# Optimization experiments

Measured on AMD Instinct MI355X. Metric: run time of the kernel, lower is better.

## Reference

```python
import jax, jax.numpy as jnp
import numpy as np

N = 100000
E = 1600000
D_IN = 128
D_H = 128
D_OUT = 40


def setup_inputs() -> dict:
    key = jax.random.key(0)
    ks = jax.random.split(key, 16)
    x = jax.random.normal(ks[0], (N, D_IN), dtype=jnp.float32)
    edge_src = jax.random.randint(ks[1], (E,), 0, N, dtype=jnp.int32)
    edge_dst = jax.random.randint(ks[2], (E,), 0, N, dtype=jnp.int32)

    def glorot(k, shape):
        fan_in, fan_out = shape[1], shape[0]
        lim = jnp.sqrt(6.0 / (fan_in + fan_out)).astype(jnp.float32)
        return jax.random.uniform(k, shape, jnp.float32, -lim, lim)

    # SAGEConv params: Wl acts on aggregated neighbors, Wr on root, plus bias.
    Wl0 = glorot(ks[3], (D_H, D_IN)); Wr0 = glorot(ks[4], (D_H, D_IN)); b0 = jnp.zeros((D_H,), jnp.float32)
    Wl1 = glorot(ks[5], (D_H, D_H));  Wr1 = glorot(ks[6], (D_H, D_H));  b1 = jnp.zeros((D_H,), jnp.float32)
    Wl2 = glorot(ks[7], (D_OUT, D_H)); Wr2 = glorot(ks[8], (D_OUT, D_H)); b2 = jnp.zeros((D_OUT,), jnp.float32)
    return {"x": x, "edge_src": edge_src, "edge_dst": edge_dst,
            "Wl0": Wl0, "Wr0": Wr0, "b0": b0,
            "Wl1": Wl1, "Wr1": Wr1, "b1": b1,
            "Wl2": Wl2, "Wr2": Wr2, "b2": b2}


def _mean_aggregate(x, edge_src, edge_dst, inv_deg):
    # adj_t @ x with mean reduce: sum neighbor feats into dst, divide by degree
    agg = jax.ops.segment_sum(x[edge_src], edge_dst, num_segments=N)
    return agg * inv_deg


def _sage_conv(x, edge_src, edge_dst, inv_deg, Wl, Wr, b):
    agg = _mean_aggregate(x, edge_src, edge_dst, inv_deg)
    return agg @ Wl.T + x @ Wr.T + b


def reference(x, edge_src, edge_dst, Wl0, Wr0, b0, Wl1, Wr1, b1, Wl2, Wr2, b2):
    deg = jax.ops.segment_sum(jnp.ones((E,), jnp.float32), edge_dst, num_segments=N)
    inv_deg = (1.0 / jnp.maximum(deg, 1.0))[:, None]  # [N,1]
    h = _sage_conv(x, edge_src, edge_dst, inv_deg, Wl0, Wr0, b0)
    h = jax.nn.relu(h)  # dropout is identity in eval mode
    h = _sage_conv(h, edge_src, edge_dst, inv_deg, Wl1, Wr1, b1)
    h = jax.nn.relu(h)
    h = _sage_conv(h, edge_src, edge_dst, inv_deg, Wl2, Wr2, b2)
    return jax.nn.log_softmax(h, axis=-1)
```

## Files before the change

kernel.cpp:

```cpp
#include <hip/hip_runtime.h>
#include <hip/hip_fp16.h>
#include <math.h>

#define NN 100000
#define NE 1600000
#define D 128
#define DOUT 40
#define NBUCK 391
#define CHUNK 4096
#define NCHUNK 391
#define LSTR 136

typedef _Float16 half8v __attribute__((ext_vector_type(8)));
typedef __attribute__((ext_vector_type(4))) float f32x4;

__device__ __forceinline__ unsigned packh(float a, float b) {
  return (unsigned)__half_as_ushort(__float2half_rn(a)) |
         ((unsigned)__half_as_ushort(__float2half_rn(b)) << 16);
}
__device__ __forceinline__ unsigned char f2fp8(float v) {
  return (unsigned char)(__builtin_amdgcn_cvt_pk_fp8_f32(v, v, 0, 0) & 0xff);
}
#define CVT2(u, s) __builtin_amdgcn_cvt_pk_f32_fp8((int)(u), s)
#define ACCR(v) { auto q = CVT2((v).x, 0); a[0] += q[0]; a[1] += q[1];   \
  q = CVT2((v).x, 1); a[2] += q[0];  a[3] += q[1];                        \
  q = CVT2((v).y, 0); a[4] += q[0];  a[5] += q[1];                        \
  q = CVT2((v).y, 1); a[6] += q[0];  a[7] += q[1];                        \
  q = CVT2((v).z, 0); a[8] += q[0];  a[9] += q[1];                        \
  q = CVT2((v).z, 1); a[10] += q[0]; a[11] += q[1];                       \
  q = CVT2((v).w, 0); a[12] += q[0]; a[13] += q[1];                       \
  q = CVT2((v).w, 1); a[14] += q[0]; a[15] += q[1]; }
#define ACCR8(v) { auto q = CVT2((v).x, 0); a[0] += q[0]; a[1] += q[1];  \
  q = CVT2((v).x, 1); a[2] += q[0]; a[3] += q[1];                         \
  q = CVT2((v).y, 0); a[4] += q[0]; a[5] += q[1];                         \
  q = CVT2((v).y, 1); a[6] += q[0]; a[7] += q[1]; }

__global__ __launch_bounds__(256) void cvt_kernel(const float* __restrict__ in,
                                                  _Float16* __restrict__ outh,
                                                  unsigned char* __restrict__ out8) {
  int i = (blockIdx.x * 256 + threadIdx.x) * 8;
  float4 v0 = *(const float4*)(in + i);
  float4 v1 = *(const float4*)(in + i + 4);
  uint4 oh;
  oh.x = packh(v0.x, v0.y);
  oh.y = packh(v0.z, v0.w);
  oh.z = packh(v1.x, v1.y);
  oh.w = packh(v1.z, v1.w);
  *(uint4*)(outh + i) = oh;
  unsigned w0 = __builtin_amdgcn_cvt_pk_fp8_f32(v0.x, v0.y, 0, 0);
  w0 = __builtin_amdgcn_cvt_pk_fp8_f32(v0.z, v0.w, w0, 1);
  unsigned w1 = __builtin_amdgcn_cvt_pk_fp8_f32(v1.x, v1.y, 0, 0);
  w1 = __builtin_amdgcn_cvt_pk_fp8_f32(v1.z, v1.w, w1, 1);
  *(uint2*)(out8 + i) = make_uint2(w0, w1);
}

__global__ __launch_bounds__(256) void bucket_hist_kernel(const int* __restrict__ dst,
                                                          int* __restrict__ bucket_cnt) {
  __shared__ int bc[NBUCK];
  int t = threadIdx.x;
  for (int i = t; i < NBUCK; i += 256) bc[i] = 0;
  __syncthreads();
  int e_base = blockIdx.x * CHUNK;
#pragma unroll
  for (int j = 0; j < 16; ++j) {
    int e = e_base + j * 256 + t;
    if (e < NE) atomicAdd(&bc[dst[e] >> 8], 1);
  }
  __syncthreads();
  for (int i = t; i < NBUCK; i += 256)
    if (bc[i]) atomicAdd(&bucket_cnt[i], bc[i]);
}

__global__ __launch_bounds__(512) void bucket_scan_kernel(const int* __restrict__ bucket_cnt,
                                                          int* __restrict__ bucket_base,
                                                          int* __restrict__ bucket_cursor) {
  __shared__ int s[512];
  int t = threadIdx.x;
  int c = (t < NBUCK) ? bucket_cnt[t] : 0;
  s[t] = c;
  __syncthreads();
  for (int off = 1; off < 512; off <<= 1) {
    int v = (t >= off) ? s[t - off] : 0;
    __syncthreads();
    s[t] += v;
    __syncthreads();
  }
  if (t < NBUCK) {
    int b = s[t] - c;
    bucket_base[t] = b;
    bucket_cursor[t] = b;
  }
  if (t == NBUCK) bucket_base[NBUCK] = s[NBUCK - 1];
}

__global__ __launch_bounds__(256) void binned_scatter_kernel(const int* __restrict__ src,
                                                             const int* __restrict__ dst,
                                                             int* __restrict__ bucket_cursor,
                                                             unsigned* __restrict__ pairs) {
  __shared__ int lcnt[NBUCK];
  __shared__ int lscan[NBUCK];
  __shared__ int gb[NBUCK];
  __shared__ unsigned ebuf[CHUNK];
  __shared__ unsigned short bbuf[CHUNK];
  int t = threadIdx.x;
  int e_base = blockIdx.x * CHUNK;
  for (int i = t; i < NBUCK; i += 256) lcnt[i] = 0;
  __syncthreads();

  int myb[16], myrank[16];
  unsigned mye[16];
#pragma unroll
  for (int j = 0; j < 16; ++j) {
    int e = e_base + j * 256 + t;
    if (e < NE) {
      int d = dst[e];
      mye[j] = (unsigned)src[e] | ((unsigned)(d & 255) << 24);
      myb[j] = d >> 8;
      myrank[j] = atomicAdd(&lcnt[d >> 8], 1);
    } else {
      myb[j] = -1;
    }
  }
  __syncthreads();

  lscan[t] = lcnt[t];
  if (256 + t < NBUCK) lscan[256 + t] = lcnt[256 + t];
  __syncthreads();
  for (int off = 1; off < 512; off <<= 1) {
    int v0 = (t >= off) ? lscan[t - off] : 0;
    int v1 = 0;
    int i1 = 256 + t;
    if (i1 < NBUCK) v1 = lscan[i1 - off];
    __syncthreads();
    if (t >= off) lscan[t] += v0;
    if (i1 < NBUCK) lscan[i1] += v1;
    __syncthreads();
  }

#pragma unroll
  for (int j = 0; j < 16; ++j)
    if (myb[j] >= 0) {
      int b = myb[j];
      int lpos = lscan[b] - lcnt[b] + myrank[j];
      ebuf[lpos] = mye[j];
      bbuf[lpos] = (unsigned short)b;
    }
  for (int i = t; i < NBUCK; i += 256)
    if (lcnt[i] > 0) gb[i] = atomicAdd(&bucket_cursor[i], lcnt[i]);
  __syncthreads();

  int chunk_n = min(CHUNK, NE - e_base);
  for (int s2 = t; s2 < chunk_n; s2 += 256) {
    int b = bbuf[s2];
    int g = gb[b] + (s2 - (lscan[b] - lcnt[b]));
    pairs[g] = ebuf[s2];
  }
}

__global__ __launch_bounds__(256) void bucket_build_kernel(const unsigned* __restrict__ pairs,
                                                           const int* __restrict__ bucket_base,
                                                           int* __restrict__ row_start,
                                                           int* __restrict__ nbr,
                                                           float* __restrict__ inv_deg) {
  __shared__ int cnt[256], loc[256], cur[256];
  int b = blockIdx.x;
  int t = threadIdx.x;
  int nbase = b << 8;
  int e0 = bucket_base[b], e1 = bucket_base[b + 1];
  cnt[t] = 0;
  __syncthreads();
  for (int e = e0 + t; e < e1; e += 256) {
    int d = (int)(pairs[e] >> 24);
    atomicAdd(&cnt[d], 1);
  }
  __syncthreads();
  loc[t] = cnt[t];
  __syncthreads();
  for (int off = 1; off < 256; off <<= 1) {
    int v = (t >= off) ? loc[t - off] : 0;
    __syncthreads();
    loc[t] += v;
    __syncthreads();
  }
  int excl = loc[t] - cnt[t];
  int node = nbase + t;
  if (node < NN) {
    row_start[node] = e0 + excl;
    inv_deg[node] = 1.0f / (float)(cnt[t] > 1 ? cnt[t] : 1);
  }
  cur[t] = excl;
  if (b == NBUCK - 1 && t == 0) row_start[NN] = NE;
  __syncthreads();
  for (int e = e0 + t; e < e1; e += 256) {
    unsigned pr = pairs[e];
    int d = (int)(pr >> 24);
    int p = atomicAdd(&cur[d], 1);
    nbr[e0 + p] = (int)(pr & 0xFFFFFFu);
  }
}

__global__ __launch_bounds__(256) void agg_kernel(const unsigned char* __restrict__ X8,
                                                  _Float16* __restrict__ out,
                                                  const int* __restrict__ row_start,
                                                  const int* __restrict__ nbr,
                                                  const float* __restrict__ inv_deg) {
  int g = blockIdx.x * 32 + (threadIdx.x >> 3);
  int ln = threadIdx.x & 7;
  if (g >= NN) return;
  int p0 = row_start[g];
  int p1 = row_start[g + 1];
  const uint4* base = (const uint4*)X8;
  float a[16];
#pragma unroll
  for (int i = 0; i < 16; ++i) a[i] = 0.f;
  int p = p0;
  for (; p + 3 < p1; p += 4) {
    int s0 = nbr[p], s1 = nbr[p + 1], s2 = nbr[p + 2], s3 = nbr[p + 3];
    uint4 v0 = base[(size_t)s0 * 8 + ln];
    uint4 v1 = base[(size_t)s1 * 8 + ln];
    uint4 v2 = base[(size_t)s2 * 8 + ln];
    uint4 v3 = base[(size_t)s3 * 8 + ln];
    ACCR(v0) ACCR(v1) ACCR(v2) ACCR(v3)
  }
  for (; p < p1; ++p) {
    uint4 v = base[(size_t)nbr[p] * 8 + ln];
    ACCR(v)
  }
  float id = inv_deg[g];
  uint4 o0, o1;
  o0.x = packh(a[0] * id, a[1] * id);
  o0.y = packh(a[2] * id, a[3] * id);
  o0.z = packh(a[4] * id, a[5] * id);
  o0.w = packh(a[6] * id, a[7] * id);
  o1.x = packh(a[8] * id, a[9] * id);
  o1.y = packh(a[10] * id, a[11] * id);
  o1.z = packh(a[12] * id, a[13] * id);
  o1.w = packh(a[14] * id, a[15] * id);
  uint4* ob = (uint4*)out;
  ob[(size_t)g * 16 + ln * 2] = o0;
  ob[(size_t)g * 16 + ln * 2 + 1] = o1;
}

__global__ __launch_bounds__(64) void prep_w_kernel(const float* __restrict__ Wl,
                                                    const float* __restrict__ Wr,
                                                    half8v* __restrict__ P) {
  int s = blockIdx.x >> 3;
  int n = blockIdx.x & 7;
  int l = threadIdx.x;
  int k0 = s * 32 + (l >> 4) * 8;
  int c = n * 16 + (l & 15);
  const float* W = (k0 < 128) ? Wl : Wr;
  int kb = (k0 < 128) ? k0 : k0 - 128;
  half8v h;
#pragma unroll
  for (int i = 0; i < 8; ++i) h[i] = (_Float16)W[c * 128 + kb + i];
  P[blockIdx.x * 64 + l] = h;
}

__global__ __launch_bounds__(64) void prep_wy2_kernel(const float* __restrict__ Wl,
                                                      const float* __restrict__ Wr,
                                                      half8v* __restrict__ P) {
  int s = blockIdx.x / 5;
  int n = blockIdx.x % 5;
  int l = threadIdx.x;
  int k0 = s * 32 + (l >> 4) * 8;
  int c = n * 16 + (l & 15);
  const float* W = (c < DOUT) ? Wl : Wr;
  int row = (c < DOUT) ? c : c - DOUT;
  half8v h;
#pragma unroll
  for (int i = 0; i < 8; ++i) h[i] = (_Float16)W[row * 128 + k0 + i];
  P[blockIdx.x * 64 + l] = h;
}

__global__ __launch_bounds__(256) void mfma_gemm_kernel(
    const _Float16* __restrict__ A, const _Float16* __restrict__ H,
    const half8v* __restrict__ B, const float* __restrict__ bias,
    _Float16* __restrict__ out, unsigned char* __restrict__ out8) {
  __shared__ _Float16 AH[2][128][LSTR];

  int t = threadIdx.x;
  int w = t >> 6, l = t & 63;
  int R0 = blockIdx.x * 128;
  int lc = l & 15;
  int lg = l >> 4;

#pragma unroll
  for (int i = 0; i < 8; ++i) {
    int u = t + 256 * i;
    int row = u >> 4, seg = u & 15;
    int gr = R0 + row;
    uint4 va = make_uint4(0, 0, 0, 0), vh = va;
    if (gr < NN) {
      va = *(const uint4*)(A + (size_t)gr * D + seg * 8);
      vh = *(const uint4*)(H + (size_t)gr * D + seg * 8);
    }
    *(uint4*)&AH[0][row][seg * 8] = va;
    *(uint4*)&AH[1][row][seg * 8] = vh;
  }
  __syncthreads();

  f32x4 acc[2][8];
#pragma unroll
  for (int m = 0; m < 2; ++m)
#pragma unroll
    for (int n = 0; n < 8; ++n) acc[m][n] = (f32x4){0.f, 0.f, 0.f, 0.f};

#pragma unroll
  for (int s = 0; s < 8; ++s) {
    int half = s >> 2;
    int koff = (s & 3) * 32;
    half8v bh[8];
#pragma unroll
    for (int n = 0; n < 8; ++n) bh[n] = B[(s * 8 + n) * 64 + l];
    half8v ah[2];
#pragma unroll
    for (int m = 0; m < 2; ++m) {
      int r = w * 32 + m * 16 + lc;
      ah[m] = *(const half8v*)&AH[half][r][koff + lg * 8];
    }
#pragma unroll
    for (int n = 0; n < 8; ++n)
#pragma unroll
      for (int m = 0; m < 2; ++m)
        acc[m][n] = __builtin_amdgcn_mfma_f32_16x16x32_f16(ah[m], bh[n], acc[m][n], 0, 0, 0);
  }

  float bcol[8];
#pragma unroll
  for (int n = 0; n < 8; ++n) bcol[n] = bias[n * 16 + lc];
#pragma unroll
  for (int m = 0; m < 2; ++m)
#pragma unroll
    for (int n = 0; n < 8; ++n) {
      int col = n * 16 + lc;
#pragma unroll
      for (int j = 0; j < 4; ++j) {
        int gr = R0 + w * 32 + m * 16 + lg * 4 + j;
        if (gr < NN) {
          float v = fmaxf(acc[m][n][j] + bcol[n], 0.f);
          out[(size_t)gr * D + col] = (_Float16)v;
          if (out8) out8[(size_t)gr * D + col] = f2fp8(v);
        }
      }
    }
}

__global__ __launch_bounds__(256) void mfma_y2_kernel(
    const _Float16* __restrict__ H, const half8v* __restrict__ B,
    const float* __restrict__ b2,
    unsigned char* __restrict__ yl8, float* __restrict__ yr) {
  __shared__ _Float16 Hs[128][LSTR];

  int t = threadIdx.x;
  int w = t >> 6, l = t & 63;
  int R0 = blockIdx.x * 128;
  int lc = l & 15;
  int lg = l >> 4;

#pragma unroll
  for (int i = 0; i < 8; ++i) {
    int u = t + 256 * i;
    int row = u >> 4, seg = u & 15;
    int gr = R0 + row;
    uint4 v = make_uint4(0, 0, 0, 0);
    if (gr < NN) v = *(const uint4*)(H + (size_t)gr * D + seg * 8);
    *(uint4*)&Hs[row][seg * 8] = v;
  }
  __syncthreads();

  f32x4 acc[2][5];
#pragma unroll
  for (int m = 0; m < 2; ++m)
#pragma unroll
    for (int n = 0; n < 5; ++n) acc[m][n] = (f32x4){0.f, 0.f, 0.f, 0.f};

#pragma unroll
  for (int s = 0; s < 4; ++s) {
    int koff = s * 32;
    half8v bh[5];
#pragma unroll
    for (int n = 0; n < 5; ++n) bh[n] = B[(s * 5 + n) * 64 + l];
    half8v ah[2];
#pragma unroll
    for (int m = 0; m < 2; ++m) {
      int r = w * 32 + m * 16 + lc;
      ah[m] = *(const half8v*)&Hs[r][koff + lg * 8];
    }
#pragma unroll
    for (int n = 0; n < 5; ++n)
#pragma unroll
      for (int m = 0; m < 2; ++m)
        acc[m][n] = __builtin_amdgcn_mfma_f32_16x16x32_f16(ah[m], bh[n], acc[m][n], 0, 0, 0);
  }

#pragma unroll
  for (int m = 0; m < 2; ++m)
#pragma unroll
    for (int n = 0; n < 5; ++n) {
      int col = n * 16 + lc;
#pragma unroll
      for (int j = 0; j < 4; ++j) {
        int gr = R0 + w * 32 + m * 16 + lg * 4 + j;
        if (gr < NN) {
          float v = acc[m][n][j];
          if (col < DOUT) {
            yl8[(size_t)gr * 48 + col] = f2fp8(v);
          } else {
            if (col < 48) yl8[(size_t)gr * 48 + col] = 0;
            yr[(size_t)gr * DOUT + (col - DOUT)] = v + b2[col - DOUT];
          }
        }
      }
    }
}

__global__ __launch_bounds__(256) void agg_out_kernel(const unsigned char* __restrict__ yl8,
                                                      const float* __restrict__ yr,
                                                      const int* __restrict__ row_start,
                                                      const int* __restrict__ nbr,
                                                      const float* __restrict__ inv_deg,
                                                      float* __restrict__ out) {
  int g = blockIdx.x * 32 + (threadIdx.x >> 3);
  int ln = threadIdx.x & 7;
  if (g >= NN) return;
  int lnc = (ln < 6) ? ln : 5;
  int p0 = row_start[g];
  int p1 = row_start[g + 1];
  const uint2* base = (const uint2*)yl8;
  float a[8];
#pragma unroll
  for (int i = 0; i < 8; ++i) a[i] = 0.f;
  int p = p0;
  for (; p + 3 < p1; p += 4) {
    int s0 = nbr[p], s1 = nbr[p + 1], s2 = nbr[p + 2], s3 = nbr[p + 3];
    uint2 v0 = base[(size_t)s0 * 6 + lnc];
    uint2 v1 = base[(size_t)s1 * 6 + lnc];
    uint2 v2 = base[(size_t)s2 * 6 + lnc];
    uint2 v3 = base[(size_t)s3 * 6 + lnc];
    ACCR8(v0) ACCR8(v1) ACCR8(v2) ACCR8(v3)
  }
  for (; p < p1; ++p) {
    uint2 v = base[(size_t)nbr[p] * 6 + lnc];
    ACCR8(v)
  }
  float id = inv_deg[g];
  float z[8];
#pragma unroll
  for (int i = 0; i < 8; ++i) z[i] = a[i] * id;
  bool valid = (ln < 5);
  if (valid) {
    float4 r0 = *(const float4*)(yr + (size_t)g * DOUT + ln * 8);
    float4 r1 = *(const float4*)(yr + (size_t)g * DOUT + ln * 8 + 4);
    z[0] += r0.x; z[1] += r0.y; z[2] += r0.z; z[3] += r0.w;
    z[4] += r1.x; z[5] += r1.y; z[6] += r1.z; z[7] += r1.w;
  }
  float zm = -INFINITY;
  if (valid)
#pragma unroll
    for (int i = 0; i < 8; ++i) zm = fmaxf(zm, z[i]);
#pragma unroll
  for (int off = 1; off < 8; off <<= 1) zm = fmaxf(zm, __shfl_xor(zm, off, 8));
  float ssum = 0.f;
  if (valid)
#pragma unroll
    for (int i = 0; i < 8; ++i) ssum += expf(z[i] - zm);
#pragma unroll
  for (int off = 1; off < 8; off <<= 1) ssum += __shfl_xor(ssum, off, 8);
  float lse = zm + logf(ssum);
  if (valid) {
    float4 o0 = make_float4(z[0] - lse, z[1] - lse, z[2] - lse, z[3] - lse);
    float4 o1 = make_float4(z[4] - lse, z[5] - lse, z[6] - lse, z[7] - lse);
    *(float4*)(out + (size_t)g * DOUT + ln * 8) = o0;
    *(float4*)(out + (size_t)g * DOUT + ln * 8 + 4) = o1;
  }
}

extern "C" void kernel_launch(void* const* d_in, const int* in_sizes, int n_in,
                              void* d_out, int out_size, void* d_ws, size_t ws_size,
                              hipStream_t stream) {
  const float* x   = (const float*)d_in[0];
  const int* esrc  = (const int*)d_in[1];
  const int* edst  = (const int*)d_in[2];
  const float* Wl0 = (const float*)d_in[3];
  const float* Wr0 = (const float*)d_in[4];
  const float* b0  = (const float*)d_in[5];
  const float* Wl1 = (const float*)d_in[6];
  const float* Wr1 = (const float*)d_in[7];
  const float* b1  = (const float*)d_in[8];
  const float* Wl2 = (const float*)d_in[9];
  const float* Wr2 = (const float*)d_in[10];
  const float* b2  = (const float*)d_in[11];
  float* out = (float*)d_out;

  char* ws = (char*)d_ws;
  size_t off = 0;
  auto carve = [&](size_t bytes) -> char* {
    char* p = ws + off;
    off = (off + bytes + 255) & ~(size_t)255;
    return p;
  };
  int* bucket_cnt    = (int*)carve((size_t)NBUCK * 4);
  int* bucket_base   = (int*)carve((size_t)(NBUCK + 1) * 4);
  int* bucket_cursor = (int*)carve((size_t)NBUCK * 4);
  int* row_start     = (int*)carve((size_t)(NN + 1) * 4);
  int* nbr           = (int*)carve((size_t)NE * 4);
  float* inv_deg     = (float*)carve((size_t)NN * 4);
  unsigned* pairs    = (unsigned*)carve((size_t)NE * 4);
  half8v* B0         = (half8v*)carve((size_t)64 * 64 * 16);
  half8v* B1         = (half8v*)carve((size_t)64 * 64 * 16);
  half8v* By2        = (half8v*)carve((size_t)20 * 64 * 16);
  _Float16* xb   = (_Float16*)carve((size_t)NN * D * 2);
  unsigned char* x8    = (unsigned char*)carve((size_t)NN * D);
  _Float16* bufA = (_Float16*)carve((size_t)NN * D * 2);
  _Float16* bufB = (_Float16*)carve((size_t)NN * D * 2);
  unsigned char* bufB8 = (unsigned char*)carve((size_t)NN * D);
  _Float16* bufC = (_Float16*)carve((size_t)NN * D * 2);
  unsigned char* yl8   = (unsigned char*)carve((size_t)NN * 48);
  float* yr      = (float*)carve((size_t)NN * DOUT * 4);
  if (off > ws_size) return;

  const int GRID_AGG = (NN + 31) / 32;
  const int GRID_GEMM = (NN + 127) / 128;
  const int GRID_CVT = NN * D / 8 / 256;
  const int GRID_AO = (NN + 31) / 32;

  hipMemsetAsync(bucket_cnt, 0, (size_t)NBUCK * 4, stream);
  bucket_hist_kernel<<<NCHUNK, 256, 0, stream>>>(edst, bucket_cnt);
  bucket_scan_kernel<<<1, 512, 0, stream>>>(bucket_cnt, bucket_base, bucket_cursor);
  binned_scatter_kernel<<<NCHUNK, 256, 0, stream>>>(esrc, edst, bucket_cursor, pairs);
  bucket_build_kernel<<<NBUCK, 256, 0, stream>>>(pairs, bucket_base, row_start, nbr, inv_deg);

  cvt_kernel<<<GRID_CVT, 256, 0, stream>>>(x, xb, x8);
  prep_w_kernel<<<64, 64, 0, stream>>>(Wl0, Wr0, B0);
  prep_w_kernel<<<64, 64, 0, stream>>>(Wl1, Wr1, B1);
  prep_wy2_kernel<<<20, 64, 0, stream>>>(Wl2, Wr2, By2);

  agg_kernel<<<GRID_AGG, 256, 0, stream>>>(x8, bufA, row_start, nbr, inv_deg);
  mfma_gemm_kernel<<<GRID_GEMM, 256, 0, stream>>>(bufA, xb, B0, b0, bufB, bufB8);
  agg_kernel<<<GRID_AGG, 256, 0, stream>>>(bufB8, bufA, row_start, nbr, inv_deg);
  mfma_gemm_kernel<<<GRID_GEMM, 256, 0, stream>>>(bufA, bufB, B1, b1, bufC, nullptr);
  mfma_y2_kernel<<<GRID_GEMM, 256, 0, stream>>>(bufC, By2, b2, yl8, yr);
  agg_out_kernel<<<GRID_AO, 256, 0, stream>>>(yl8, yr, row_start, nbr, inv_deg, out);
}
```

Before: 261.7 us.

## Load GEMM A-fragments directly from global and stage outputs through LDS for coalesced stores

Both MFMA kernels stop staging the input tiles in shared memory and instead load each lane's A fragments straight from global memory, clamping row indices so no bounds check is needed. The epilogues now write results into an LDS tile and then store them with vectorised, coalesced row writes; the fp8 copy is derived from the staged fp16 values. This replaces scattered 2-byte and 1-byte global stores and frees LDS, which can raise occupancy. The memset is also replaced by a tiny zeroing kernel. Direct fragment loads are less coalesced than the old tile load, and converting fp8 from fp16 adds a second rounding step.

New measurement: 231.7 us. 1.13x faster.

```diff
diff --git a/kernel.cpp b/kernel.cpp
--- a/kernel.cpp
+++ b/kernel.cpp
@@ -34,6 +34,11 @@
   q = CVT2((v).x, 1); a[2] += q[0]; a[3] += q[1];                         \
   q = CVT2((v).y, 0); a[4] += q[0]; a[5] += q[1];                         \
   q = CVT2((v).y, 1); a[6] += q[0]; a[7] += q[1]; }
+
+__global__ void zero_kernel(int* __restrict__ p, int n) {
+  int i = blockIdx.x * 256 + threadIdx.x;
+  if (i < n) p[i] = 0;
+}
 
 __global__ __launch_bounds__(256) void cvt_kernel(const float* __restrict__ in,
                                                   _Float16* __restrict__ outh,
@@ -277,7 +282,7 @@
     const _Float16* __restrict__ A, const _Float16* __restrict__ H,
     const half8v* __restrict__ B, const float* __restrict__ bias,
     _Float16* __restrict__ out, unsigned char* __restrict__ out8) {
-  __shared__ _Float16 AH[2][128][LSTR];
+  __shared__ _Float16 Os[128][LSTR];
 
   int t = threadIdx.x;
   int w = t >> 6, l = t & 63;
@@ -285,72 +290,81 @@
   int lc = l & 15;
   int lg = l >> 4;
 
+  int frow = R0 + w * 32 + lc;
+  int fr0 = min(frow, NN - 1);
+  int fr1 = min(frow + 16, NN - 1);
+
+  f32x4 acc[2][8];
+#pragma unroll
+  for (int m = 0; m < 2; ++m)
+#pragma unroll
+    for (int n = 0; n < 8; ++n) acc[m][n] = (f32x4){0.f, 0.f, 0.f, 0.f};
+
+#pragma unroll
+  for (int s = 0; s < 8; ++s) {
+    const _Float16* src = (s < 4) ? A : H;
+    int koff = (s & 3) * 32 + lg * 8;
+    half8v ah0 = *(const half8v*)(src + (size_t)fr0 * D + koff);
+    half8v ah1 = *(const half8v*)(src + (size_t)fr1 * D + koff);
+    half8v bh[8];
+#pragma unroll
+    for (int n = 0; n < 8; ++n) bh[n] = B[(s * 8 + n) * 64 + l];
+#pragma unroll
+    for (int n = 0; n < 8; ++n) {
+      acc[0][n] = __builtin_amdgcn_mfma_f32_16x16x32_f16(ah0, bh[n], acc[0][n], 0, 0, 0);
+      acc[1][n] = __builtin_amdgcn_mfma_f32_16x16x32_f16(ah1, bh[n], acc[1][n], 0, 0, 0);
+    }
+  }
+
+  float bcol[8];
+#pragma unroll
+  for (int n = 0; n < 8; ++n) bcol[n] = bias[n * 16 + lc];
+#pragma unroll
+  for (int m = 0; m < 2; ++m)
+#pragma unroll
+    for (int n = 0; n < 8; ++n) {
+      int col = n * 16 + lc;
+#pragma unroll
+      for (int j = 0; j < 4; ++j) {
+        int row = w * 32 + m * 16 + lg * 4 + j;
+        Os[row][col] = (_Float16)fmaxf(acc[m][n][j] + bcol[n], 0.f);
+      }
+    }
+  __syncthreads();
+
 #pragma unroll
   for (int i = 0; i < 8; ++i) {
     int u = t + 256 * i;
     int row = u >> 4, seg = u & 15;
     int gr = R0 + row;
-    uint4 va = make_uint4(0, 0, 0, 0), vh = va;
     if (gr < NN) {
-      va = *(const uint4*)(A + (size_t)gr * D + seg * 8);
-      vh = *(const uint4*)(H + (size_t)gr * D + seg * 8);
-    }
-    *(uint4*)&AH[0][row][seg * 8] = va;
-    *(uint4*)&AH[1][row][seg * 8] = vh;
-  }
-  __syncthreads();
-
-  f32x4 acc[2][8];
-#pragma unroll
-  for (int m = 0; m < 2; ++m)
-#pragma unroll
-    for (int n = 0; n < 8; ++n) acc[m][n] = (f32x4){0.f, 0.f, 0.f, 0.f};
-
-#pragma unroll
-  for (int s = 0; s < 8; ++s) {
-    int half = s >> 2;
-    int koff = (s & 3) * 32;
-    half8v bh[8];
-#pragma unroll
-    for (int n = 0; n < 8; ++n) bh[n] = B[(s * 8 + n) * 64 + l];
-    half8v ah[2];
-#pragma unroll
-    for (int m = 0; m < 2; ++m) {
-      int r = w * 32 + m * 16 + lc;
-      ah[m] = *(const half8v*)&AH[half][r][koff + lg * 8];
-    }
-#pragma unroll
-    for (int n = 0; n < 8; ++n)
-#pragma unroll
-      for (int m = 0; m < 2; ++m)
-        acc[m][n] = __builtin_amdgcn_mfma_f32_16x16x32_f16(ah[m], bh[n], acc[m][n], 0, 0, 0);
-  }
-
-  float bcol[8];
-#pragma unroll
-  for (int n = 0; n < 8; ++n) bcol[n] = bias[n * 16 + lc];
-#pragma unroll
-  for (int m = 0; m < 2; ++m)
-#pragma unroll
-    for (int n = 0; n < 8; ++n) {
-      int col = n * 16 + lc;
-#pragma unroll
-      for (int j = 0; j < 4; ++j) {
-        int gr = R0 + w * 32 + m * 16 + lg * 4 + j;
-        if (gr < NN) {
-          float v = fmaxf(acc[m][n][j] + bcol[n], 0.f);
-          out[(size_t)gr * D + col] = (_Float16)v;
-          if (out8) out8[(size_t)gr * D + col] = f2fp8(v);
-        }
+      uint4 v = *(const uint4*)&Os[row][seg * 8];
+      *(uint4*)(out + (size_t)gr * D + seg * 8) = v;
+      if (out8) {
+        unsigned w0 = __builtin_amdgcn_cvt_pk_fp8_f32(
+            __half2float(__ushort_as_half((unsigned short)(v.x & 0xffff))),
+            __half2float(__ushort_as_half((unsigned short)(v.x >> 16))), 0, 0);
+        w0 = __builtin_amdgcn_cvt_pk_fp8_f32(
+            __half2float(__ushort_as_half((unsigned short)(v.y & 0xffff))),
+            __half2float(__ushort_as_half((unsigned short)(v.y >> 16))), w0, 1);
+        unsigned w1 = __builtin_amdgcn_cvt_pk_fp8_f32(
+            __half2float(__ushort_as_half((unsigned short)(v.z & 0xffff))),
+            __half2float(__ushort_as_half((unsigned short)(v.z >> 16))), 0, 0);
+        w1 = __builtin_amdgcn_cvt_pk_fp8_f32(
+            __half2float(__ushort_as_half((unsigned short)(v.w & 0xffff))),
+            __half2float(__ushort_as_half((unsigned short)(v.w >> 16))), w1, 1);
+        *(uint2*)(out8 + (size_t)gr * D + seg * 8) = make_uint2(w0, w1);
       }
     }
+  }
 }
 
 __global__ __launch_bounds__(256) void mfma_y2_kernel(
     const _Float16* __restrict__ H, const half8v* __restrict__ B,
     const float* __restrict__ b2,
     unsigned char* __restrict__ yl8, float* __restrict__ yr) {
-  __shared__ _Float16 Hs[128][LSTR];
+  __shared__ unsigned char Y8[128][48];
+  __shared__ float Yr[128][40];
 
   int t = threadIdx.x;
   int w = t >> 6, l = t & 63;
@@ -358,16 +372,9 @@
   int lc = l & 15;
   int lg = l >> 4;
 
-#pragma unroll
-  for (int i = 0; i < 8; ++i) {
-    int u = t + 256 * i;
-    int row = u >> 4, seg = u & 15;
-    int gr = R0 + row;
-    uint4 v = make_uint4(0, 0, 0, 0);
-    if (gr < NN) v = *(const uint4*)(H + (size_t)gr * D + seg * 8);
-    *(uint4*)&Hs[row][seg * 8] = v;
-  }
-  __syncthreads();
+  int frow = R0 + w * 32 + lc;
+  int fr0 = min(frow, NN - 1);
+  int fr1 = min(frow + 16, NN - 1);
 
   f32x4 acc[2][5];
 #pragma unroll
@@ -377,21 +384,17 @@
 
 #pragma unroll
   for (int s = 0; s < 4; ++s) {
-    int koff = s * 32;
+    int koff = s * 32 + lg * 8;
+    half8v ah0 = *(const half8v*)(H + (size_t)fr0 * D + koff);
+    half8v ah1 = *(const half8v*)(H + (size_t)fr1 * D + koff);
     half8v bh[5];
 #pragma unroll
     for (int n = 0; n < 5; ++n) bh[n] = B[(s * 5 + n) * 64 + l];
-    half8v ah[2];
-#pragma unroll
-    for (int m = 0; m < 2; ++m) {
-      int r = w * 32 + m * 16 + lc;
-      ah[m] = *(const half8v*)&Hs[r][koff + lg * 8];
-    }
-#pragma unroll
-    for (int n = 0; n < 5; ++n)
-#pragma unroll
-      for (int m = 0; m < 2; ++m)
-        acc[m][n] = __builtin_amdgcn_mfma_f32_16x16x32_f16(ah[m], bh[n], acc[m][n], 0, 0, 0);
+#pragma unroll
+    for (int n = 0; n < 5; ++n) {
+      acc[0][n] = __builtin_amdgcn_mfma_f32_16x16x32_f16(ah0, bh[n], acc[0][n], 0, 0, 0);
+      acc[1][n] = __builtin_amdgcn_mfma_f32_16x16x32_f16(ah1, bh[n], acc[1][n], 0, 0, 0);
+    }
   }
 
 #pragma unroll
@@ -401,18 +404,32 @@
       int col = n * 16 + lc;
 #pragma unroll
       for (int j = 0; j < 4; ++j) {
-        int gr = R0 + w * 32 + m * 16 + lg * 4 + j;
-        if (gr < NN) {
-          float v = acc[m][n][j];
-          if (col < DOUT) {
-            yl8[(size_t)gr * 48 + col] = f2fp8(v);
-          } else {
-            if (col < 48) yl8[(size_t)gr * 48 + col] = 0;
-            yr[(size_t)gr * DOUT + (col - DOUT)] = v + b2[col - DOUT];
-          }
+        int row = w * 32 + m * 16 + lg * 4 + j;
+        float v = acc[m][n][j];
+        if (col < DOUT) {
+          Y8[row][col] = f2fp8(v);
+        } else {
+          Yr[row][col - DOUT] = v + b2[col - DOUT];
         }
       }
     }
+  if (t < 128) *(uint2*)&Y8[t][40] = make_uint2(0, 0);
+  __syncthreads();
+
+#pragma unroll
+  for (int i = 0; i < 3; ++i) {
+    int u = t + 256 * i;
+    int row = u / 6, seg = u % 6;
+    int gr = R0 + row;
+    if (gr < NN) *(uint2*)(yl8 + (size_t)gr * 48 + seg * 8) = *(const uint2*)&Y8[row][seg * 8];
+  }
+#pragma unroll
+  for (int i = 0; i < 5; ++i) {
+    int u = t + 256 * i;
+    int row = u / 10, seg = u % 10;
+    int gr = R0 + row;
+    if (gr < NN) *(float4*)(yr + (size_t)gr * DOUT + seg * 4) = *(const float4*)&Yr[row][seg * 4];
+  }
 }
 
 __global__ __launch_bounds__(256) void agg_out_kernel(const unsigned char* __restrict__ yl8,
@@ -525,7 +542,7 @@
   const int GRID_CVT = NN * D / 8 / 256;
   const int GRID_AO = (NN + 31) / 32;
 
-  hipMemsetAsync(bucket_cnt, 0, (size_t)NBUCK * 4, stream);
+  zero_kernel<<<2, 256, 0, stream>>>(bucket_cnt, NBUCK);
   bucket_hist_kernel<<<NCHUNK, 256, 0, stream>>>(edst, bucket_cnt);
   bucket_scan_kernel<<<1, 512, 0, stream>>>(bucket_cnt, bucket_base, bucket_cursor);
   binned_scatter_kernel<<<NCHUNK, 256, 0, stream>>>(esrc, edst, bucket_cursor, pairs);
```
